# Kernel tuning notes

Hardware: AMD Instinct MI355X
Metric: run time of the kernel (lower is better)

The kernel has to match this reference:

```python
import jax, jax.numpy as jnp
import numpy as np

B, S, D, H = 2, 2048, 512, 8
DK = D // H


def setup_inputs() -> dict:
    key = jax.random.key(0)
    ks = jax.random.split(key, 6)
    q = jax.random.normal(ks[0], (B, S, D), dtype=jnp.float32)
    k = jax.random.normal(ks[1], (B, S, D), dtype=jnp.float32)
    v = jax.random.normal(ks[2], (B, S, D), dtype=jnp.float32)
    mask = jax.random.randint(ks[3], (1, 1, S, S), 0, 2, dtype=jnp.int32)
    # nn.Linear weights [out, in]; scaled like torch default init
    Wq = jax.random.normal(ks[4], (D, D), dtype=jnp.float32) / np.sqrt(D)
    Wo = jax.random.normal(ks[5], (D, D), dtype=jnp.float32) / np.sqrt(D)
    return {"q": q, "k": k, "v": v, "mask": mask, "Wq": Wq, "Wo": Wo}


def _split_heads(x):
    # [B,S,D] -> [B,H,S,DK]
    return x.reshape(B, S, H, DK).transpose(0, 2, 1, 3)


def reference(q, k, v, mask, Wq, Wo):
    # NOTE: original module applies Wq to q, k AND v (faithful to source bug)
    query = _split_heads(q @ Wq.T)
    key_ = _split_heads(k @ Wq.T)
    value = _split_heads(v @ Wq.T)
    scores = jnp.einsum("bhqd,bhkd->bhqk", query, key_) / np.sqrt(DK).astype(np.float32)
    # original uses masked_fill_(mask==0, 1e-09) BEFORE softmax (not -inf)
    scores = jnp.where(mask == 0, jnp.float32(1e-9), scores)
    attn = jax.nn.softmax(scores, axis=-1)  # dropout p=0.0 -> identity
    x = jnp.einsum("bhqk,bhkd->bhqd", attn, value)
    x = x.transpose(0, 2, 1, 3).reshape(B, S, D)
    return x @ Wo.T
```

## Files before the change

kernel.cpp:

```cpp
#include <hip/hip_runtime.h>
#include <hip/hip_bf16.h>
#include <stdint.h>

#define S_LEN 2048
#define D_MOD 512
#define N_H   8
#define D_K   64

typedef short v8s __attribute__((ext_vector_type(8)));
typedef short v4s __attribute__((ext_vector_type(4)));
typedef float v4f __attribute__((ext_vector_type(4)));

__device__ __forceinline__ short f2bf(float f) {
  union { float f; unsigned u; } a; a.f = f;
  unsigned u = a.u;
  u += 0x7fffu + ((u >> 16) & 1u);
  return (short)(u >> 16);
}

__device__ __forceinline__ v4f mfma16(v8s a, v8s b, v4f c) {
  return __builtin_amdgcn_mfma_f32_16x16x32_bf16(a, b, c, 0, 0, 0);
}
__device__ __forceinline__ v4f mfma16x16(v4s a, v4s b, v4f c) {
  return __builtin_amdgcn_mfma_f32_16x16x16bf16_1k(a, b, c, 0, 0, 0);
}

__global__ __launch_bounds__(256) void prep_kernel(
    const float* __restrict__ q, const float* __restrict__ k,
    const float* __restrict__ v, const float* __restrict__ Wq,
    const float* __restrict__ Wo, const int* __restrict__ mask,
    short* __restrict__ qb, short* __restrict__ kb, short* __restrict__ vb,
    short* __restrict__ Wqb, short* __restrict__ Wob,
    unsigned long long* __restrict__ mp)
{
  unsigned bx = blockIdx.x;
  if (bx < 6656u) {
    unsigned g = bx * 256 + threadIdx.x;
    const float* src; short* dst; unsigned off;
    if (g < 524288u)        { src = q;  dst = qb;  off = g; }
    else if (g < 1048576u)  { src = k;  dst = kb;  off = g - 524288u; }
    else if (g < 1572864u)  { src = v;  dst = vb;  off = g - 1048576u; }
    else if (g < 1638400u)  { src = Wq; dst = Wqb; off = g - 1572864u; }
    else                    { src = Wo; dst = Wob; off = g - 1638400u; }
    float4 x = ((const float4*)src)[off];
    v4s p; p.x = f2bf(x.x); p.y = f2bf(x.y); p.z = f2bf(x.z); p.w = f2bf(x.w);
    ((v4s*)dst)[off] = p;
  } else {
    int id = (bx - 6656u) * 256 + threadIdx.x;
    const int4* m4 = (const int4*)(mask + (size_t)id * 64);
    unsigned long long w = 0ull;
#pragma unroll
    for (int j = 0; j < 16; j++) {
      int4 mv = m4[j];
      w |= (unsigned long long)(mv.x != 0) << (j * 4 + 0);
      w |= (unsigned long long)(mv.y != 0) << (j * 4 + 1);
      w |= (unsigned long long)(mv.z != 0) << (j * 4 + 2);
      w |= (unsigned long long)(mv.w != 0) << (j * 4 + 3);
    }
    mp[id] = w;
  }
}

__global__ __launch_bounds__(256) void proj_kernel(
    const short* __restrict__ qb, const short* __restrict__ kb,
    const short* __restrict__ vb, const short* __restrict__ Wqb,
    short* __restrict__ QP, short* __restrict__ KP, short* __restrict__ VT)
{
  const int z = blockIdx.z;
  const short* __restrict__ A = (z == 0) ? qb : ((z == 1) ? kb : vb);
  const int m0 = blockIdx.x * 64, n0 = blockIdx.y * 64;
  const int tid = threadIdx.x;
  const int wave = tid >> 6, lane = tid & 63;
  const int quad = lane >> 4, l15 = lane & 15;
  const int wm = wave >> 1, wn = wave & 1;
  __shared__ short As[64][72];
  __shared__ short Bs[64][72];
  v4f acc[2][2];
#pragma unroll
  for (int i = 0; i < 2; i++)
#pragma unroll
    for (int j = 0; j < 2; j++) acc[i][j] = (v4f){0.f, 0.f, 0.f, 0.f};

  v8s a8[2], b8[2];
#pragma unroll
  for (int i = 0; i < 2; i++) {
    int fi = tid + i * 256, r = fi >> 3, c = (fi & 7) << 3;
    a8[i] = *(const v8s*)&A[(m0 + r) * 512 + c];
    b8[i] = *(const v8s*)&Wqb[(n0 + r) * 512 + c];
  }

  for (int kk = 0; kk < 512; kk += 64) {
    __syncthreads();
#pragma unroll
    for (int i = 0; i < 2; i++) {
      int fi = tid + i * 256, r = fi >> 3, c = (fi & 7) << 3;
      *(v8s*)&As[r][c] = a8[i];
      *(v8s*)&Bs[r][c] = b8[i];
    }
    __syncthreads();
    if (kk + 64 < 512) {
#pragma unroll
      for (int i = 0; i < 2; i++) {
        int fi = tid + i * 256, r = fi >> 3, c = (fi & 7) << 3;
        a8[i] = *(const v8s*)&A[(m0 + r) * 512 + kk + 64 + c];
        b8[i] = *(const v8s*)&Wqb[(n0 + r) * 512 + kk + 64 + c];
      }
    }
#pragma unroll
    for (int ms = 0; ms < 2; ms++)
#pragma unroll
      for (int ns = 0; ns < 2; ns++)
#pragma unroll
        for (int ks = 0; ks < 2; ks++) {
          union { v8s v; v4s h2[2]; } a, bb;
          a.h2[0]  = *(const v4s*)&As[wm * 32 + ms * 16 + l15][ks * 32 + quad * 8];
          a.h2[1]  = *(const v4s*)&As[wm * 32 + ms * 16 + l15][ks * 32 + quad * 8 + 4];
          bb.h2[0] = *(const v4s*)&Bs[wn * 32 + ns * 16 + l15][ks * 32 + quad * 8];
          bb.h2[1] = *(const v4s*)&Bs[wn * 32 + ns * 16 + l15][ks * 32 + quad * 8 + 4];
          acc[ms][ns] = mfma16(a.v, bb.v, acc[ms][ns]);
        }
  }
#pragma unroll
  for (int ms = 0; ms < 2; ms++)
#pragma unroll
    for (int ns = 0; ns < 2; ns++) {
      int mb = m0 + wm * 32 + ms * 16 + quad * 4;
      int n  = n0 + wn * 32 + ns * 16 + l15;
      int bI = mb >> 11, s = mb & 2047, hh = n >> 6, dk = n & 63;
      if (z == 2) {
        v4s pv;
        pv.x = f2bf(acc[ms][ns][0]); pv.y = f2bf(acc[ms][ns][1]);
        pv.z = f2bf(acc[ms][ns][2]); pv.w = f2bf(acc[ms][ns][3]);
        *(v4s*)&VT[((bI * N_H + hh) * D_K + dk) * S_LEN + s] = pv;
      } else {
        short* dst = (z == 0) ? QP : KP;
#pragma unroll
        for (int r = 0; r < 4; r++)
          dst[((bI * N_H + hh) * S_LEN + (s + r)) * D_K + dk] = f2bf(acc[ms][ns][r]);
      }
    }
}

__global__ __launch_bounds__(512, 4) void attn_kernel(
    const short* __restrict__ QP, const short* __restrict__ KP,
    const short* __restrict__ VT, const unsigned long long* __restrict__ mp,
    short* __restrict__ XP)
{
  const int h = blockIdx.y, b = blockIdx.z;
  const int tid = threadIdx.x;
  const int wave = tid >> 6;
  const int half = wave >> 2;
  const int wq   = wave & 3;
  const int lane = tid & 63;
  const int quad = lane >> 4, l15 = lane & 15;
  const short* Qh = QP + ((b * N_H + h) * S_LEN) * D_K;
  const short* Kh = KP + ((b * N_H + h) * S_LEN) * D_K;
  const short* Vh = VT + ((b * N_H + h) * D_K) * S_LEN;

  __shared__ char smem[36864];
  short* Ks = (short*)smem + half * 4608;
  short* Vs = (short*)(smem + 18432) + half * 4608;
  float* CB = (float*)smem;

  const int qrow = blockIdx.x * 64 + wq * 16;
  const int t8   = tid & 255;
  const int srow = t8 >> 2;
  const int sc   = (t8 & 3) * 8;
  const int ch0  = half * 1024;

  v8s aQ[2];
#pragma unroll
  for (int ks = 0; ks < 2; ks++)
    aQ[ks] = *(const v8s*)&Qh[(qrow + l15) * D_K + ks * 32 + quad * 8];

  const float MASKP = 3.3546263e-4f;
  float lacc = 0.f;
  v4f accX[4];
#pragma unroll
  for (int u = 0; u < 4; u++) accX[u] = (v4f){0.f, 0.f, 0.f, 0.f};

  v8s kreg0 = *(const v8s*)&Kh[(ch0 + srow) * D_K + sc];
  v8s kreg1 = *(const v8s*)&Kh[(ch0 + srow) * D_K + sc + 32];
  v8s vreg0 = *(const v8s*)&Vh[srow * S_LEN + ch0 + sc];
  v8s vreg1 = *(const v8s*)&Vh[srow * S_LEN + ch0 + sc + 32];
  unsigned long long mwc = mp[(qrow + l15) * 32 + half * 16];
  unsigned long long mwn = 0ull;

  for (int kt = 0; kt < 16; kt++) {
    __syncthreads();
    *(v8s*)&Ks[srow * 72 + sc]      = kreg0;
    *(v8s*)&Ks[srow * 72 + sc + 32] = kreg1;
    *(v8s*)&Vs[srow * 72 + sc]      = vreg0;
    *(v8s*)&Vs[srow * 72 + sc + 32] = vreg1;
    __syncthreads();

    if (kt + 1 < 16) {
      const int c1 = ch0 + (kt + 1) * 64;
      kreg0 = *(const v8s*)&Kh[(c1 + srow) * D_K + sc];
      kreg1 = *(const v8s*)&Kh[(c1 + srow) * D_K + sc + 32];
      vreg0 = *(const v8s*)&Vh[srow * S_LEN + c1 + sc];
      vreg1 = *(const v8s*)&Vh[srow * S_LEN + c1 + sc + 32];
      mwn = mp[(qrow + l15) * 32 + half * 16 + kt + 1];
    }

    v4s pa[4];
#pragma unroll
    for (int tp = 0; tp < 4; tp++) {
      v4f s = (v4f){0.f, 0.f, 0.f, 0.f};
#pragma unroll
      for (int ks = 0; ks < 2; ks++) {
        v8s bK = *(const v8s*)&Ks[(tp * 16 + l15) * 72 + ks * 32 + quad * 8];
        s = mfma16(bK, aQ[ks], s);
      }
      v4s pk;
#pragma unroll
      for (int r = 0; r < 4; r++) {
        int kap = tp * 16 + quad * 4 + r;
        int bit = (int)((mwc >> kap) & 1ull);
        float p = bit ? __expf(fmaf(s[r], 0.125f, -8.0f)) : MASKP;
        lacc += p;
        pk[r] = f2bf(p);
      }
      pa[tp] = pk;
    }

#pragma unroll
    for (int u = 0; u < 4; u++) {
      const short* vb_ = &Vs[(u * 16 + l15) * 72 + quad * 4];
#pragma unroll
      for (int tp = 0; tp < 4; tp++) {
        v4s bV = *(const v4s*)&vb_[tp * 16];
        accX[u] = mfma16x16(pa[tp], bV, accX[u]);
      }
    }
    mwc = mwn;
  }

  lacc += __shfl_xor(lacc, 16);
  lacc += __shfl_xor(lacc, 32);

  __syncthreads();
  if (half == 1) {
    float* c = CB + (wq * 64 + lane) * 17;
#pragma unroll
    for (int u = 0; u < 4; u++)
#pragma unroll
      for (int r = 0; r < 4; r++) c[u * 4 + r] = accX[u][r];
    c[16] = lacc;
  }
  __syncthreads();
  if (half == 0) {
    const float* c = CB + (wq * 64 + lane) * 17;
#pragma unroll
    for (int u = 0; u < 4; u++)
#pragma unroll
      for (int r = 0; r < 4; r++) accX[u][r] += c[u * 4 + r];
    float lsum = lacc + c[16];
    float inv[4];
#pragma unroll
    for (int r = 0; r < 4; r++)
      inv[r] = 1.0f / __shfl(lsum, quad * 4 + r);
#pragma unroll
    for (int u = 0; u < 4; u++)
#pragma unroll
      for (int r = 0; r < 4; r++) {
        float x = accX[u][r] * inv[r];
        int srw = qrow + quad * 4 + r;
        XP[(b * S_LEN + srw) * D_MOD + h * D_K + u * 16 + l15] = f2bf(x);
      }
  }
}

__global__ __launch_bounds__(256) void outproj_kernel(
    const short* __restrict__ XP, const short* __restrict__ Wob,
    float* __restrict__ out)
{
  const int m0 = blockIdx.x * 64, n0 = blockIdx.y * 64;
  const int tid = threadIdx.x;
  const int wave = tid >> 6, lane = tid & 63;
  const int quad = lane >> 4, l15 = lane & 15;
  const int wm = wave >> 1, wn = wave & 1;
  __shared__ short As[64][72];
  __shared__ short Bs[64][72];
  v4f acc[2][2];
#pragma unroll
  for (int i = 0; i < 2; i++)
#pragma unroll
    for (int j = 0; j < 2; j++) acc[i][j] = (v4f){0.f, 0.f, 0.f, 0.f};

  v8s a8[2], b8[2];
#pragma unroll
  for (int i = 0; i < 2; i++) {
    int fi = tid + i * 256, r = fi >> 3, c = (fi & 7) << 3;
    a8[i] = *(const v8s*)&XP[(m0 + r) * 512 + c];
    b8[i] = *(const v8s*)&Wob[(n0 + r) * 512 + c];
  }

  for (int kk = 0; kk < 512; kk += 64) {
    __syncthreads();
#pragma unroll
    for (int i = 0; i < 2; i++) {
      int fi = tid + i * 256, r = fi >> 3, c = (fi & 7) << 3;
      *(v8s*)&As[r][c] = a8[i];
      *(v8s*)&Bs[r][c] = b8[i];
    }
    __syncthreads();
    if (kk + 64 < 512) {
#pragma unroll
      for (int i = 0; i < 2; i++) {
        int fi = tid + i * 256, r = fi >> 3, c = (fi & 7) << 3;
        a8[i] = *(const v8s*)&XP[(m0 + r) * 512 + kk + 64 + c];
        b8[i] = *(const v8s*)&Wob[(n0 + r) * 512 + kk + 64 + c];
      }
    }
#pragma unroll
    for (int ms = 0; ms < 2; ms++)
#pragma unroll
      for (int ns = 0; ns < 2; ns++)
#pragma unroll
        for (int ks = 0; ks < 2; ks++) {
          union { v8s v; v4s h2[2]; } a, bb;
          a.h2[0]  = *(const v4s*)&As[wm * 32 + ms * 16 + l15][ks * 32 + quad * 8];
          a.h2[1]  = *(const v4s*)&As[wm * 32 + ms * 16 + l15][ks * 32 + quad * 8 + 4];
          bb.h2[0] = *(const v4s*)&Bs[wn * 32 + ns * 16 + l15][ks * 32 + quad * 8];
          bb.h2[1] = *(const v4s*)&Bs[wn * 32 + ns * 16 + l15][ks * 32 + quad * 8 + 4];
          acc[ms][ns] = mfma16(a.v, bb.v, acc[ms][ns]);
        }
  }
#pragma unroll
  for (int ms = 0; ms < 2; ms++)
#pragma unroll
    for (int ns = 0; ns < 2; ns++) {
      int n = n0 + wn * 32 + ns * 16 + l15;
#pragma unroll
      for (int r = 0; r < 4; r++) {
        int m = m0 + wm * 32 + ms * 16 + quad * 4 + r;
        out[m * 512 + n] = acc[ms][ns][r];
      }
    }
}

extern "C" void kernel_launch(void* const* d_in, const int* in_sizes, int n_in,
                              void* d_out, int out_size, void* d_ws, size_t ws_size,
                              hipStream_t stream) {
  const float* q  = (const float*)d_in[0];
  const float* k  = (const float*)d_in[1];
  const float* v  = (const float*)d_in[2];
  const int* mask = (const int*)d_in[3];
  const float* Wq = (const float*)d_in[4];
  const float* Wo = (const float*)d_in[5];
  float* out = (float*)d_out;
  char* ws = (char*)d_ws;
  short* QP = (short*)(ws);
  short* KP = (short*)(ws + (4u << 20));
  short* VT = (short*)(ws + (8u << 20));
  short* XP = (short*)(ws + (12u << 20));
  unsigned long long* MP = (unsigned long long*)(ws + (16u << 20));
  short* qb  = (short*)(ws + (17u << 20));
  short* kb  = (short*)(ws + (21u << 20));
  short* vb  = (short*)(ws + (25u << 20));
  short* Wqb = (short*)(ws + (29u << 20));
  short* Wob = (short*)(ws + (29u << 20) + (512u << 10));

  prep_kernel<<<dim3(6912), 256, 0, stream>>>(q, k, v, Wq, Wo, mask,
                                              qb, kb, vb, Wqb, Wob, MP);
  proj_kernel<<<dim3(64, 8, 3), 256, 0, stream>>>(qb, kb, vb, Wqb, QP, KP, VT);
  attn_kernel<<<dim3(32, N_H, 2), 512, 0, stream>>>(QP, KP, VT, MP, XP);
  outproj_kernel<<<dim3(64, 8, 1), 256, 0, stream>>>(XP, Wob, out);
}
```

Before: 163.8 us.

## Fuse fp32-to-bf16 conversion into projection and restructure attention into four key groups

Removes the separate prep kernel: the projection GEMM now loads fp32 q/k/v/Wq directly and converts to bf16 while staging into shared memory, and an extra z-slice packs the mask and converts Wo. The attention kernel splits keys across four wave groups that each process two 16-row query tiles, sharing K/V loads across both tiles. Row sums are computed with an MFMA against a ones vector. Softmax now uses exp2 with folded constants and a cheaper bf16 rounding. This cuts one launch and a global round-trip of the bf16 copies, at the cost of twice the shared memory, a four-way reduction, and redundant fp32 reads and conversions across GEMM tiles.

```diff
diff --git a/kernel.cpp b/kernel.cpp
--- a/kernel.cpp
+++ b/kernel.cpp
@@ -17,6 +17,10 @@
   u += 0x7fffu + ((u >> 16) & 1u);
   return (short)(u >> 16);
 }
+__device__ __forceinline__ short f2bfh(float f) {
+  union { float f; unsigned u; } a; a.f = f;
+  return (short)((a.u + 0x8000u) >> 16);
+}
 
 __device__ __forceinline__ v4f mfma16(v8s a, v8s b, v4f c) {
   return __builtin_amdgcn_mfma_f32_16x16x32_bf16(a, b, c, 0, 0, 0);
@@ -25,51 +29,40 @@
   return __builtin_amdgcn_mfma_f32_16x16x16bf16_1k(a, b, c, 0, 0, 0);
 }
 
-__global__ __launch_bounds__(256) void prep_kernel(
+__global__ __launch_bounds__(256) void proj_kernel(
     const float* __restrict__ q, const float* __restrict__ k,
     const float* __restrict__ v, const float* __restrict__ Wq,
     const float* __restrict__ Wo, const int* __restrict__ mask,
-    short* __restrict__ qb, short* __restrict__ kb, short* __restrict__ vb,
-    short* __restrict__ Wqb, short* __restrict__ Wob,
-    unsigned long long* __restrict__ mp)
-{
-  unsigned bx = blockIdx.x;
-  if (bx < 6656u) {
-    unsigned g = bx * 256 + threadIdx.x;
-    const float* src; short* dst; unsigned off;
-    if (g < 524288u)        { src = q;  dst = qb;  off = g; }
-    else if (g < 1048576u)  { src = k;  dst = kb;  off = g - 524288u; }
-    else if (g < 1572864u)  { src = v;  dst = vb;  off = g - 1048576u; }
-    else if (g < 1638400u)  { src = Wq; dst = Wqb; off = g - 1572864u; }
-    else                    { src = Wo; dst = Wob; off = g - 1638400u; }
-    float4 x = ((const float4*)src)[off];
-    v4s p; p.x = f2bf(x.x); p.y = f2bf(x.y); p.z = f2bf(x.z); p.w = f2bf(x.w);
-    ((v4s*)dst)[off] = p;
-  } else {
-    int id = (bx - 6656u) * 256 + threadIdx.x;
-    const int4* m4 = (const int4*)(mask + (size_t)id * 64);
-    unsigned long long w = 0ull;
-#pragma unroll
-    for (int j = 0; j < 16; j++) {
-      int4 mv = m4[j];
-      w |= (unsigned long long)(mv.x != 0) << (j * 4 + 0);
-      w |= (unsigned long long)(mv.y != 0) << (j * 4 + 1);
-      w |= (unsigned long long)(mv.z != 0) << (j * 4 + 2);
-      w |= (unsigned long long)(mv.w != 0) << (j * 4 + 3);
-    }
-    mp[id] = w;
-  }
-}
-
-__global__ __launch_bounds__(256) void proj_kernel(
-    const short* __restrict__ qb, const short* __restrict__ kb,
-    const short* __restrict__ vb, const short* __restrict__ Wqb,
-    short* __restrict__ QP, short* __restrict__ KP, short* __restrict__ VT)
+    short* __restrict__ QP, short* __restrict__ KP, short* __restrict__ VT,
+    short* __restrict__ Wob, unsigned long long* __restrict__ mp)
 {
   const int z = blockIdx.z;
-  const short* __restrict__ A = (z == 0) ? qb : ((z == 1) ? kb : vb);
+  const int tid = threadIdx.x;
+  if (z == 3) {
+    int bid = blockIdx.x * 8 + blockIdx.y;
+    if (bid < 256) {
+      int id = bid * 256 + tid;
+      const int4* m4 = (const int4*)(mask + (size_t)id * 64);
+      unsigned long long w = 0ull;
+#pragma unroll
+      for (int j = 0; j < 16; j++) {
+        int4 mv = m4[j];
+        w |= (unsigned long long)(mv.x != 0) << (j * 4 + 0);
+        w |= (unsigned long long)(mv.y != 0) << (j * 4 + 1);
+        w |= (unsigned long long)(mv.z != 0) << (j * 4 + 2);
+        w |= (unsigned long long)(mv.w != 0) << (j * 4 + 3);
+      }
+      mp[id] = w;
+    } else {
+      unsigned off = (bid - 256) * 256 + tid;
+      float4 x = ((const float4*)Wo)[off];
+      v4s p; p.x = f2bf(x.x); p.y = f2bf(x.y); p.z = f2bf(x.z); p.w = f2bf(x.w);
+      ((v4s*)Wob)[off] = p;
+    }
+    return;
+  }
+  const float* __restrict__ A = (z == 0) ? q : ((z == 1) ? k : v);
   const int m0 = blockIdx.x * 64, n0 = blockIdx.y * 64;
-  const int tid = threadIdx.x;
   const int wave = tid >> 6, lane = tid & 63;
   const int quad = lane >> 4, l15 = lane & 15;
   const int wm = wave >> 1, wn = wave & 1;
@@ -81,29 +74,31 @@
 #pragma unroll
     for (int j = 0; j < 2; j++) acc[i][j] = (v4f){0.f, 0.f, 0.f, 0.f};
 
-  v8s a8[2], b8[2];
-#pragma unroll
-  for (int i = 0; i < 2; i++) {
-    int fi = tid + i * 256, r = fi >> 3, c = (fi & 7) << 3;
-    a8[i] = *(const v8s*)&A[(m0 + r) * 512 + c];
-    b8[i] = *(const v8s*)&Wqb[(n0 + r) * 512 + c];
+  float4 a4[4], b4[4];
+#pragma unroll
+  for (int i = 0; i < 4; i++) {
+    int fi = tid + i * 256, r = fi >> 4, c = (fi & 15) << 2;
+    a4[i] = *(const float4*)&A[(m0 + r) * 512 + c];
+    b4[i] = *(const float4*)&Wq[(n0 + r) * 512 + c];
   }
 
   for (int kk = 0; kk < 512; kk += 64) {
     __syncthreads();
 #pragma unroll
-    for (int i = 0; i < 2; i++) {
-      int fi = tid + i * 256, r = fi >> 3, c = (fi & 7) << 3;
-      *(v8s*)&As[r][c] = a8[i];
-      *(v8s*)&Bs[r][c] = b8[i];
+    for (int i = 0; i < 4; i++) {
+      int fi = tid + i * 256, r = fi >> 4, c = (fi & 15) << 2;
+      v4s ap; ap.x = f2bf(a4[i].x); ap.y = f2bf(a4[i].y); ap.z = f2bf(a4[i].z); ap.w = f2bf(a4[i].w);
+      *(v4s*)&As[r][c] = ap;
+      v4s bp; bp.x = f2bf(b4[i].x); bp.y = f2bf(b4[i].y); bp.z = f2bf(b4[i].z); bp.w = f2bf(b4[i].w);
+      *(v4s*)&Bs[r][c] = bp;
     }
     __syncthreads();
     if (kk + 64 < 512) {
 #pragma unroll
-      for (int i = 0; i < 2; i++) {
-        int fi = tid + i * 256, r = fi >> 3, c = (fi & 7) << 3;
-        a8[i] = *(const v8s*)&A[(m0 + r) * 512 + kk + 64 + c];
-        b8[i] = *(const v8s*)&Wqb[(n0 + r) * 512 + kk + 64 + c];
+      for (int i = 0; i < 4; i++) {
+        int fi = tid + i * 256, r = fi >> 4, c = (fi & 15) << 2;
+        a4[i] = *(const float4*)&A[(m0 + r) * 512 + kk + 64 + c];
+        b4[i] = *(const float4*)&Wq[(n0 + r) * 512 + kk + 64 + c];
       }
     }
 #pragma unroll
@@ -149,79 +144,94 @@
   const int h = blockIdx.y, b = blockIdx.z;
   const int tid = threadIdx.x;
   const int wave = tid >> 6;
-  const int half = wave >> 2;
-  const int wq   = wave & 3;
+  const int grp  = wave >> 1;
+  const int wg   = wave & 1;
   const int lane = tid & 63;
   const int quad = lane >> 4, l15 = lane & 15;
   const short* Qh = QP + ((b * N_H + h) * S_LEN) * D_K;
   const short* Kh = KP + ((b * N_H + h) * S_LEN) * D_K;
   const short* Vh = VT + ((b * N_H + h) * D_K) * S_LEN;
 
-  __shared__ char smem[36864];
-  short* Ks = (short*)smem + half * 4608;
-  short* Vs = (short*)(smem + 18432) + half * 4608;
+  __shared__ char smem[73728];
+  short* Ks = (short*)smem + grp * 4608;
+  short* Vs = (short*)(smem + 36864) + grp * 4608;
   float* CB = (float*)smem;
 
-  const int qrow = blockIdx.x * 64 + wq * 16;
-  const int t8   = tid & 255;
-  const int srow = t8 >> 2;
-  const int sc   = (t8 & 3) * 8;
-  const int ch0  = half * 1024;
-
-  v8s aQ[2];
-#pragma unroll
-  for (int ks = 0; ks < 2; ks++)
-    aQ[ks] = *(const v8s*)&Qh[(qrow + l15) * D_K + ks * 32 + quad * 8];
-
-  const float MASKP = 3.3546263e-4f;
-  float lacc = 0.f;
-  v4f accX[4];
-#pragma unroll
-  for (int u = 0; u < 4; u++) accX[u] = (v4f){0.f, 0.f, 0.f, 0.f};
-
-  v8s kreg0 = *(const v8s*)&Kh[(ch0 + srow) * D_K + sc];
-  v8s kreg1 = *(const v8s*)&Kh[(ch0 + srow) * D_K + sc + 32];
-  v8s vreg0 = *(const v8s*)&Vh[srow * S_LEN + ch0 + sc];
-  v8s vreg1 = *(const v8s*)&Vh[srow * S_LEN + ch0 + sc + 32];
-  unsigned long long mwc = mp[(qrow + l15) * 32 + half * 16];
-  unsigned long long mwn = 0ull;
-
-  for (int kt = 0; kt < 16; kt++) {
-    __syncthreads();
-    *(v8s*)&Ks[srow * 72 + sc]      = kreg0;
-    *(v8s*)&Ks[srow * 72 + sc + 32] = kreg1;
-    *(v8s*)&Vs[srow * 72 + sc]      = vreg0;
-    *(v8s*)&Vs[srow * 72 + sc + 32] = vreg1;
-    __syncthreads();
-
-    if (kt + 1 < 16) {
-      const int c1 = ch0 + (kt + 1) * 64;
-      kreg0 = *(const v8s*)&Kh[(c1 + srow) * D_K + sc];
-      kreg1 = *(const v8s*)&Kh[(c1 + srow) * D_K + sc + 32];
-      vreg0 = *(const v8s*)&Vh[srow * S_LEN + c1 + sc];
-      vreg1 = *(const v8s*)&Vh[srow * S_LEN + c1 + sc + 32];
-      mwn = mp[(qrow + l15) * 32 + half * 16 + kt + 1];
-    }
-
-    v4s pa[4];
+  const int qrow0 = blockIdx.x * 64 + wg * 32;
+  const int t128 = tid & 127;
+  const int srow = t128 >> 1;
+  const int sc   = (t128 & 1) * 32;
+  const int ck0  = grp * 512;
+
+  v8s aQ[2][2];
+#pragma unroll
+  for (int g = 0; g < 2; g++)
+#pragma unroll
+    for (int ks = 0; ks < 2; ks++)
+      aQ[g][ks] = *(const v8s*)&Qh[(qrow0 + g * 16 + l15) * D_K + ks * 32 + quad * 8];
+
+  const float C1 = 0.18033688011112042f;
+  const float C2 = -11.541560327111707f;
+  const v4s ONES4 = {16256, 16256, 16256, 16256};
+  v4f accX[2][4], accL[2];
+#pragma unroll
+  for (int g = 0; g < 2; g++) {
+    accL[g] = (v4f){0.f, 0.f, 0.f, 0.f};
+#pragma unroll
+    for (int u = 0; u < 4; u++) accX[g][u] = (v4f){0.f, 0.f, 0.f, 0.f};
+  }
+
+  v8s kr[4], vr[4];
+#pragma unroll
+  for (int j = 0; j < 4; j++) {
+    kr[j] = *(const v8s*)&Kh[(ck0 + srow) * D_K + sc + j * 8];
+    vr[j] = *(const v8s*)&Vh[srow * S_LEN + ck0 + sc + j * 8];
+  }
+  unsigned long long mwc[2], mwn[2] = {0ull, 0ull};
+#pragma unroll
+  for (int g = 0; g < 2; g++)
+    mwc[g] = mp[(qrow0 + g * 16 + l15) * 32 + grp * 8];
+
+  for (int kt = 0; kt < 8; kt++) {
+    __syncthreads();
+#pragma unroll
+    for (int j = 0; j < 4; j++) {
+      *(v8s*)&Ks[srow * 72 + sc + j * 8] = kr[j];
+      *(v8s*)&Vs[srow * 72 + sc + j * 8] = vr[j];
+    }
+    __syncthreads();
+
+    if (kt + 1 < 8) {
+      const int c1 = ck0 + (kt + 1) * 64;
+#pragma unroll
+      for (int j = 0; j < 4; j++) {
+        kr[j] = *(const v8s*)&Kh[(c1 + srow) * D_K + sc + j * 8];
+        vr[j] = *(const v8s*)&Vh[srow * S_LEN + c1 + sc + j * 8];
+      }
+#pragma unroll
+      for (int g = 0; g < 2; g++)
+        mwn[g] = mp[(qrow0 + g * 16 + l15) * 32 + grp * 8 + kt + 1];
+    }
+
+    v4s pa[2][4];
 #pragma unroll
     for (int tp = 0; tp < 4; tp++) {
-      v4f s = (v4f){0.f, 0.f, 0.f, 0.f};
-#pragma unroll
-      for (int ks = 0; ks < 2; ks++) {
-        v8s bK = *(const v8s*)&Ks[(tp * 16 + l15) * 72 + ks * 32 + quad * 8];
-        s = mfma16(bK, aQ[ks], s);
-      }
-      v4s pk;
-#pragma unroll
-      for (int r = 0; r < 4; r++) {
-        int kap = tp * 16 + quad * 4 + r;
-        int bit = (int)((mwc >> kap) & 1ull);
-        float p = bit ? __expf(fmaf(s[r], 0.125f, -8.0f)) : MASKP;
-        lacc += p;
-        pk[r] = f2bf(p);
-      }
-      pa[tp] = pk;
+      v8s bK0 = *(const v8s*)&Ks[(tp * 16 + l15) * 72 + quad * 8];
+      v8s bK1 = *(const v8s*)&Ks[(tp * 16 + l15) * 72 + 32 + quad * 8];
+#pragma unroll
+      for (int g = 0; g < 2; g++) {
+        v4f s = mfma16(bK0, aQ[g][0], (v4f){0.f, 0.f, 0.f, 0.f});
+        s = mfma16(bK1, aQ[g][1], s);
+        unsigned mb = (unsigned)(mwc[g] >> (tp * 16 + quad * 4));
+        v4s pk;
+#pragma unroll
+        for (int r = 0; r < 4; r++) {
+          float se = ((mb >> r) & 1u) ? s[r] : 0.0f;
+          float p = __builtin_amdgcn_exp2f(fmaf(se, C1, C2));
+          pk[r] = f2bfh(p);
+        }
+        pa[g][tp] = pk;
+      }
     }
 
 #pragma unroll
@@ -230,44 +240,61 @@
 #pragma unroll
       for (int tp = 0; tp < 4; tp++) {
         v4s bV = *(const v4s*)&vb_[tp * 16];
-        accX[u] = mfma16x16(pa[tp], bV, accX[u]);
-      }
-    }
-    mwc = mwn;
-  }
-
-  lacc += __shfl_xor(lacc, 16);
-  lacc += __shfl_xor(lacc, 32);
+        accX[0][u] = mfma16x16(pa[0][tp], bV, accX[0][u]);
+        accX[1][u] = mfma16x16(pa[1][tp], bV, accX[1][u]);
+      }
+    }
+#pragma unroll
+    for (int g = 0; g < 2; g++)
+#pragma unroll
+      for (int tp = 0; tp < 4; tp++)
+        accL[g] = mfma16x16(pa[g][tp], ONES4, accL[g]);
+
+    mwc[0] = mwn[0]; mwc[1] = mwn[1];
+  }
 
   __syncthreads();
-  if (half == 1) {
-    float* c = CB + (wq * 64 + lane) * 17;
-#pragma unroll
-    for (int u = 0; u < 4; u++)
-#pragma unroll
-      for (int r = 0; r < 4; r++) c[u * 4 + r] = accX[u][r];
-    c[16] = lacc;
+  if (grp > 0) {
+    float* c = CB + ((grp - 1) * 128 + t128) * 41;
+#pragma unroll
+    for (int g = 0; g < 2; g++) {
+#pragma unroll
+      for (int u = 0; u < 4; u++)
+#pragma unroll
+        for (int r = 0; r < 4; r++) c[(g * 4 + u) * 4 + r] = accX[g][u][r];
+#pragma unroll
+      for (int r = 0; r < 4; r++) c[32 + g * 4 + r] = accL[g][r];
+    }
   }
   __syncthreads();
-  if (half == 0) {
-    const float* c = CB + (wq * 64 + lane) * 17;
-#pragma unroll
-    for (int u = 0; u < 4; u++)
-#pragma unroll
-      for (int r = 0; r < 4; r++) accX[u][r] += c[u * 4 + r];
-    float lsum = lacc + c[16];
-    float inv[4];
-#pragma unroll
-    for (int r = 0; r < 4; r++)
-      inv[r] = 1.0f / __shfl(lsum, quad * 4 + r);
-#pragma unroll
-    for (int u = 0; u < 4; u++)
-#pragma unroll
-      for (int r = 0; r < 4; r++) {
-        float x = accX[u][r] * inv[r];
-        int srw = qrow + quad * 4 + r;
-        XP[(b * S_LEN + srw) * D_MOD + h * D_K + u * 16 + l15] = f2bf(x);
-      }
+  if (grp == 0) {
+#pragma unroll
+    for (int w = 0; w < 3; w++) {
+      const float* c = CB + (w * 128 + t128) * 41;
+#pragma unroll
+      for (int g = 0; g < 2; g++) {
+#pragma unroll
+        for (int u = 0; u < 4; u++)
+#pragma unroll
+          for (int r = 0; r < 4; r++) accX[g][u][r] += c[(g * 4 + u) * 4 + r];
+#pragma unroll
+        for (int r = 0; r < 4; r++) accL[g][r] += c[32 + g * 4 + r];
+      }
+    }
+#pragma unroll
+    for (int g = 0; g < 2; g++) {
+      float inv[4];
+#pragma unroll
+      for (int r = 0; r < 4; r++) inv[r] = 1.0f / accL[g][r];
+#pragma unroll
+      for (int u = 0; u < 4; u++)
+#pragma unroll
+        for (int r = 0; r < 4; r++) {
+          int srw = qrow0 + g * 16 + quad * 4 + r;
+          XP[(b * S_LEN + srw) * D_MOD + h * D_K + u * 16 + l15] =
+              f2bf(accX[g][u][r] * inv[r]);
+        }
+    }
   }
 }
 
@@ -356,15 +383,10 @@
   short* VT = (short*)(ws + (8u << 20));
   short* XP = (short*)(ws + (12u << 20));
   unsigned long long* MP = (unsigned long long*)(ws + (16u << 20));
-  short* qb  = (short*)(ws + (17u << 20));
-  short* kb  = (short*)(ws + (21u << 20));
-  short* vb  = (short*)(ws + (25u << 20));
-  short* Wqb = (short*)(ws + (29u << 20));
-  short* Wob = (short*)(ws + (29u << 20) + (512u << 10));
-
-  prep_kernel<<<dim3(6912), 256, 0, stream>>>(q, k, v, Wq, Wo, mask,
-                                              qb, kb, vb, Wqb, Wob, MP);
-  proj_kernel<<<dim3(64, 8, 3), 256, 0, stream>>>(qb, kb, vb, Wqb, QP, KP, VT);
+  short* Wob = (short*)(ws + (16u << 20) + (512u << 10));
+
+  proj_kernel<<<dim3(64, 8, 4), 256, 0, stream>>>(q, k, v, Wq, Wo, mask,
+                                                  QP, KP, VT, Wob, MP);
   attn_kernel<<<dim3(32, N_H, 2), 512, 0, stream>>>(QP, KP, VT, MP, XP);
   outproj_kernel<<<dim3(64, 8, 1), 256, 0, stream>>>(XP, Wob, out);
 }
```

Measured after the change: 151.9 us. 1.08x faster.
